# Optimization experiments

Hardware: AMD Instinct MI355X
Metric: run time of the kernel (lower is better)

The kernel has to match this reference:

```python
import jax, jax.numpy as jnp
import numpy as np

N = 50000      # nodes
E = 300000     # edges per relation
IN = 128       # in_feats
HF = 64        # h_feats
AH = 4         # att_heads
R = 3          # relations
H = HF * AH    # 256, per-relation hidden width


def setup_inputs() -> dict:
    key = jax.random.key(0)
    ks = jax.random.split(key, 10)
    s = 0.05
    h = jax.random.normal(ks[0], (N, IN), jnp.float32)
    # relation_aware params (shared across relations)
    dW = jax.random.normal(ks[1], (IN, H), jnp.float32) * s
    db = jnp.zeros((H,), jnp.float32)
    fW = jax.random.normal(ks[2], (3 * H, 1), jnp.float32) * s
    fb = jnp.zeros((1,), jnp.float32)
    # per-relation H2FDLayer params (stacked over R)
    wW = jax.random.normal(ks[3], (R, IN, H), jnp.float32) * s
    wb = jnp.zeros((R, H), jnp.float32)
    aW = jax.random.normal(ks[4], (R, 2 * HF, 1), jnp.float32) * s
    ab = jnp.zeros((R, 1), jnp.float32)
    # final combining linear
    linW = jax.random.normal(ks[5], (R * H, H), jnp.float32) * s
    linb = jnp.zeros((H,), jnp.float32)
    src = jax.random.randint(ks[6], (R, E), 0, N, jnp.int32)
    dst = jax.random.randint(ks[7], (R, E), 0, N, jnp.int32)
    return dict(h=h, dW=dW, db=db, fW=fW, fb=fb, wW=wW, wb=wb,
                aW=aW, ab=ab, linW=linW, linb=linb, src=src, dst=dst)


def _segment_softmax(alpha, seg, num_segments):
    # alpha: [E, AH]; softmax over edges sharing the same destination node
    amax = jax.ops.segment_max(alpha, seg, num_segments=num_segments)
    ex = jnp.exp(alpha - amax[seg])
    denom = jax.ops.segment_sum(ex, seg, num_segments=num_segments)
    return ex / denom[seg]


def reference(h, dW, db, fW, fb, wW, wb, aW, ab, linW, linb, src, dst):
    hd = h @ dW + db  # [N, H] relation_aware d_liner (shared)
    outs = []
    for r in range(R):
        s_idx, d_idx = src[r], dst[r]
        sd, dd = hd[s_idx], hd[d_idx]  # [E, H]
        # sign_edges: tanh(f_liner(cat[src,dst,src-dst])) -> sign
        score = jnp.tanh((jnp.concatenate([sd, dd, sd - dd], axis=1) @ fW + fb)[:, 0])
        sign = jnp.sign(score)  # [E]
        hw = h @ wW[r] + wb[r]  # [N, H] per-relation w_liner
        sf = (sign[:, None] * hw[s_idx]).reshape(E, AH, HF)          # signed src features
        z = jnp.concatenate([sf, hw[d_idx].reshape(E, AH, HF)], -1)  # [E, AH, 2*HF]
        alpha = jax.nn.leaky_relu((z @ aW[r] + ab[r])[..., 0], 0.01)  # [E, AH]
        w = _segment_softmax(alpha, d_idx, N)                         # [E, AH]
        out_r = jax.ops.segment_sum(w[..., None] * sf, d_idx, num_segments=N)
        outs.append(out_r.reshape(N, H))
    out = jnp.concatenate(outs, axis=1)  # [N, R*H]
    return out @ linW + linb             # [N, H]
```

## Files before the change

kernel.cpp:

```cpp
#include <hip/hip_runtime.h>

#define NN 50000
#define MP 50048
#define EE 300000
#define KIN 128
#define HH 256
#define KOUT 768
#define NAH 4
#define NHF 64
#define NR 3

#define GSH 7
#define NG 391
#define NBKT (NR * NG)
#define BCAP 1024
#define EPB 16384
#define NTOT (NR * EE)

typedef __attribute__((ext_vector_type(8))) short short8_t;
typedef __attribute__((ext_vector_type(4))) float f32x4;

#define O_DBL   0ull
#define O_GS    4096ull
#define O_GD    204096ull
#define O_ASRC  404096ull
#define O_ADST  2804096ull
#define O_GCNT  5204096ull
#define O_GBUF  5212288ull
#define O_H16   10016896ull
#define O_WT    22829184ull
#define O_LWT   23025792ull
#define O_HW16  23419008ull
#define O_OUTA  100292736ull
#define NEED_A  177166464ull

__device__ __forceinline__ ushort f2bf(float x) {
  union { float f; unsigned u; } c; c.f = x;
  return (ushort)((c.u + 0x7FFFu + ((c.u >> 16) & 1u)) >> 16);
}
__device__ __forceinline__ float bf2f(ushort u) {
  return __uint_as_float(((unsigned)u) << 16);
}

__global__ void k_prep(const float* __restrict__ dW, const float* __restrict__ db,
                       const float* __restrict__ fW, double* __restrict__ dbuf) {
  int t = threadIdx.x;
  if (t < KIN) {
    double p = 0.0, q = 0.0;
    for (int j = 0; j < HH; ++j) {
      double u = (double)fW[j] + (double)fW[2 * HH + j];
      double v = (double)fW[HH + j] - (double)fW[2 * HH + j];
      double w = (double)dW[t * HH + j];
      p += w * u; q += w * v;
    }
    dbuf[t] = p; dbuf[KIN + t] = q;
  } else if (t == KIN) {
    double cu = 0.0, cv = 0.0;
    for (int j = 0; j < HH; ++j) {
      double u = (double)fW[j] + (double)fW[2 * HH + j];
      double v = (double)fW[HH + j] - (double)fW[2 * HH + j];
      cu += (double)db[j] * u; cv += (double)db[j] * v;
    }
    dbuf[2 * KIN] = cu; dbuf[2 * KIN + 1] = cv;
  }
}

__global__ __launch_bounds__(256) void k_gsgd(const float* __restrict__ h,
                                              const double* __restrict__ dbuf,
                                              float* __restrict__ gs, float* __restrict__ gd) {
  int node = (int)((blockIdx.x * 256u + threadIdx.x) >> 6);
  int lane = threadIdx.x & 63;
  if (node >= NN) return;
  float2 hv = *(const float2*)&h[(size_t)node * KIN + lane * 2];
  double ps = (double)hv.x * dbuf[lane * 2] + (double)hv.y * dbuf[lane * 2 + 1];
  double qs = (double)hv.x * dbuf[KIN + lane * 2] + (double)hv.y * dbuf[KIN + lane * 2 + 1];
#pragma unroll
  for (int m = 32; m; m >>= 1) { ps += __shfl_xor(ps, m, 64); qs += __shfl_xor(qs, m, 64); }
  if (lane == 0) {
    gs[node] = (float)(ps + dbuf[2 * KIN]);
    gd[node] = (float)(qs + dbuf[2 * KIN + 1]);
  }
}

__global__ __launch_bounds__(256) void k_cvtA(const float* __restrict__ h, ushort* __restrict__ h16) {
  int t = blockIdx.x * 256 + threadIdx.x;
  if (t >= MP * KIN / 8) return;
  int row = t >> 4, c8 = (t & 15) * 8;
  ushort o[8];
  if (row < NN) {
    float4 v0 = *(const float4*)&h[(size_t)row * KIN + c8];
    float4 v1 = *(const float4*)&h[(size_t)row * KIN + c8 + 4];
    o[0] = f2bf(v0.x); o[1] = f2bf(v0.y); o[2] = f2bf(v0.z); o[3] = f2bf(v0.w);
    o[4] = f2bf(v1.x); o[5] = f2bf(v1.y); o[6] = f2bf(v1.z); o[7] = f2bf(v1.w);
  } else {
#pragma unroll
    for (int i = 0; i < 8; ++i) o[i] = 0;
  }
  *(short8_t*)&h16[(size_t)row * KIN + c8] = *(short8_t*)o;
}

#define WT_ELEMS (NR * HH * KIN)
#define LWT_ELEMS (HH * KOUT)
__global__ __launch_bounds__(256) void k_cvtW(const float* __restrict__ wW, const float* __restrict__ linW,
                                              ushort* __restrict__ Wt, ushort* __restrict__ LWt) {
  int t = blockIdx.x * 256 + threadIdx.x;
  if (t < WT_ELEMS) {
    int r = t / (HH * KIN), rem = t % (HH * KIN);
    int n = rem / KIN, k = rem % KIN;
    Wt[t] = f2bf(wW[((size_t)r * KIN + k) * HH + n]);
  }
  int u = t - WT_ELEMS;
  if (u >= 0 && u < LWT_ELEMS) {
    int n = u / KOUT, kk = u % KOUT;
    LWt[u] = f2bf(linW[(size_t)kk * HH + n]);
  }
}

template <int K, bool ACC, bool BIAS, bool OBF16>
__global__ __launch_bounds__(256) void k_mm(const ushort* __restrict__ A0,
                                            const ushort* __restrict__ Bt0,
                                            const float* __restrict__ bias0,
                                            void* __restrict__ Cv, int M, int bStride,
                                            size_t aZ, size_t btZ, size_t biasZ, size_t cZ) {
  __shared__ ushort As[128][40];
  __shared__ ushort Bs[128][40];
  const ushort* A = A0 + (size_t)blockIdx.z * aZ;
  const ushort* Bt = Bt0 + (size_t)blockIdx.z * btZ;
  const float* bias = BIAS ? bias0 + (size_t)blockIdx.z * biasZ : bias0;
  size_t cOfs = (size_t)blockIdx.z * cZ;
  int bm = blockIdx.x * 128, bn = blockIdx.y * 128;
  int tid = threadIdx.x, lane = tid & 63, w = tid >> 6;
  int wm = w >> 1, wn = w & 1;
  int sr = tid >> 2, sk = (tid & 3) * 8;
  int fr = lane & 15, kb = (lane >> 4) * 8;
  f32x4 acc[4][4] = {};
  for (int k0 = 0; k0 < K; k0 += 32) {
    short8_t a0 = *(const short8_t*)&A[(size_t)(bm + sr) * K + k0 + sk];
    short8_t a1 = *(const short8_t*)&A[(size_t)(bm + 64 + sr) * K + k0 + sk];
    short8_t b0 = *(const short8_t*)&Bt[(size_t)(bn + sr) * bStride + k0 + sk];
    short8_t b1 = *(const short8_t*)&Bt[(size_t)(bn + 64 + sr) * bStride + k0 + sk];
    __syncthreads();
    *(short8_t*)&As[sr][sk] = a0;
    *(short8_t*)&As[64 + sr][sk] = a1;
    *(short8_t*)&Bs[sr][sk] = b0;
    *(short8_t*)&Bs[64 + sr][sk] = b1;
    __syncthreads();
    short8_t af[4], bfr[4];
#pragma unroll
    for (int i = 0; i < 4; ++i) af[i] = *(const short8_t*)&As[wm * 64 + i * 16 + fr][kb];
#pragma unroll
    for (int i = 0; i < 4; ++i) bfr[i] = *(const short8_t*)&Bs[wn * 64 + i * 16 + fr][kb];
#pragma unroll
    for (int i = 0; i < 4; ++i)
#pragma unroll
      for (int j = 0; j < 4; ++j)
        acc[i][j] = __builtin_amdgcn_mfma_f32_16x16x32_bf16(af[i], bfr[j], acc[i][j], 0, 0, 0);
  }
  int rq = lane >> 4;
#pragma unroll
  for (int i = 0; i < 4; ++i) {
#pragma unroll
    for (int j = 0; j < 4; ++j) {
      int col = bn + wn * 64 + j * 16 + fr;
      float bv = 0.f;
      if constexpr (BIAS) bv = bias[col];
#pragma unroll
      for (int q = 0; q < 4; ++q) {
        int row = bm + wm * 64 + i * 16 + rq * 4 + q;
        if (row < M) {
          float v = acc[i][j][q] + bv;
          if constexpr (OBF16) {
            ((ushort*)Cv)[cOfs + (size_t)row * HH + col] = f2bf(v);
          } else {
            float* C = (float*)Cv;
            if constexpr (ACC) v += C[(size_t)row * HH + col];
            C[(size_t)row * HH + col] = v;
          }
        }
      }
    }
  }
}

__global__ __launch_bounds__(256) void k_aproj(const ushort* __restrict__ hwAll, size_t hwZ,
                                               const float* __restrict__ aWAll,
                                               float* __restrict__ asrcAll, float* __restrict__ adstAll,
                                               int rbase) {
  int r = rbase + blockIdx.y;
  const ushort* hw = hwAll + (size_t)(blockIdx.y) * hwZ;
  const float* aW = aWAll + (size_t)r * 2 * NHF;
  int node = (int)((blockIdx.x * 256u + threadIdx.x) >> 6);
  int lane = threadIdx.x & 63;
  if (node >= NN) return;
  int ah = lane >> 4, j = lane & 15;
  ushort4 hv4 = *(const ushort4*)&hw[(size_t)node * HH + ah * NHF + j * 4];
  float hx = bf2f(hv4.x), hy = bf2f(hv4.y), hz = bf2f(hv4.z), hwv = bf2f(hv4.w);
  float4 a1 = *(const float4*)&aW[j * 4];
  float4 a2 = *(const float4*)&aW[NHF + j * 4];
  float s1 = hx * a1.x + hy * a1.y + hz * a1.z + hwv * a1.w;
  float s2 = hx * a2.x + hy * a2.y + hz * a2.z + hwv * a2.w;
#pragma unroll
  for (int m = 8; m; m >>= 1) { s1 += __shfl_xor(s1, m, 64); s2 += __shfl_xor(s2, m, 64); }
  if (j == 0) {
    asrcAll[(size_t)r * NN * NAH + node * NAH + ah] = s1;
    adstAll[(size_t)r * NN * NAH + node * NAH + ah] = s2;
  }
}

__global__ __launch_bounds__(512) void k_bin(const int* __restrict__ dst,
                                             int* __restrict__ gcnt,
                                             uint* __restrict__ gbuf) {
  __shared__ int hist[NBKT];
  __shared__ int base[NBKT];
  int tid = threadIdx.x;
  int start = blockIdx.x * EPB;
  for (int b = tid; b < NBKT; b += 512) hist[b] = 0;
  __syncthreads();
#pragma unroll 4
  for (int i = 0; i < EPB / 512; ++i) {
    int e = start + i * 512 + tid;
    if (e < NTOT) {
      int d = dst[e];
      int r = (e >= 2 * EE) ? 2 : ((e >= EE) ? 1 : 0);
      atomicAdd(&hist[r * NG + (d >> GSH)], 1);
    }
  }
  __syncthreads();
  for (int b = tid; b < NBKT; b += 512) {
    int c = hist[b];
    base[b] = (c > 0) ? atomicAdd(&gcnt[b], c) : 0;
    hist[b] = 0;
  }
  __syncthreads();
#pragma unroll 4
  for (int i = 0; i < EPB / 512; ++i) {
    int e = start + i * 512 + tid;
    if (e < NTOT) {
      int d = dst[e];
      int r = (e >= 2 * EE) ? 2 : ((e >= EE) ? 1 : 0);
      int bkt = r * NG + (d >> GSH);
      int idx = base[bkt] + atomicAdd(&hist[bkt], 1);
      if (idx < BCAP)
        gbuf[(size_t)bkt * BCAP + idx] = ((uint)(d & 127) << 19) | (uint)(e - r * EE);
    }
  }
}

__global__ __launch_bounds__(512) void k_edgeB(const int* __restrict__ srcAll,
                                               const ushort* __restrict__ hwAll, size_t hwZ,
                                               const float* __restrict__ gs,
                                               const float* __restrict__ gd,
                                               const float* __restrict__ asrcAll,
                                               const float* __restrict__ adstAll,
                                               const float* __restrict__ fb,
                                               const float* __restrict__ abAll,
                                               const int* __restrict__ gcnt,
                                               const uint* __restrict__ gbuf,
                                               ushort* __restrict__ outB,
                                               int outStride, int colMul, int rbase) {
  __shared__ uint ebuf[BCAP];
  __shared__ uint csr[BCAP];
  __shared__ int cntL[128], offL[128], curL[128];
  int rl = blockIdx.x / NG, g = blockIdx.x % NG;
  int r = rbase + rl;
  const int* src = srcAll + (size_t)r * EE;
  const ushort* hw = hwAll + (size_t)rl * hwZ;
  const float* asrc = asrcAll + (size_t)r * NN * NAH;
  const float* adst = adstAll + (size_t)r * NN * NAH;
  int bkt = r * NG + g;
  int tid = threadIdx.x;
  int cb = gcnt[bkt]; if (cb > BCAP) cb = BCAP;
  if (tid < 128) { cntL[tid] = 0; curL[tid] = 0; }
  __syncthreads();
  for (int i = tid; i < cb; i += 512) {
    uint ent = gbuf[(size_t)bkt * BCAP + i];
    ebuf[i] = ent;
    atomicAdd(&cntL[ent >> 19], 1);
  }
  __syncthreads();
  if (tid < 64) {
    int c0 = cntL[2 * tid], c1 = cntL[2 * tid + 1];
    int s = c0 + c1, inc = s;
#pragma unroll
    for (int o = 1; o < 64; o <<= 1) {
      int v = __shfl_up(inc, o, 64);
      if (tid >= o) inc += v;
    }
    int ex = inc - s;
    offL[2 * tid] = ex;
    offL[2 * tid + 1] = ex + c0;
  }
  __syncthreads();
  for (int i = tid; i < cb; i += 512) {
    uint ent = ebuf[i];
    int b = (int)(ent >> 19);
    int idx = atomicAdd(&curL[b], 1);
    csr[offL[b] + idx] = ent;
  }
  __syncthreads();

  int lane = tid & 63, wv = tid >> 6;
  int head = lane >> 4, iE = lane >> 2, cah = lane & 3;
  float fbv = fb[0], abv = abAll[r];
  int colBase = colMul * r * HH + lane * 4;
  for (int it = 0; it < 16; ++it) {
    int ln = wv + 8 * it;
    int node = (g << GSH) + ln;
    if (node >= NN) continue;
    int deg = cntL[ln]; deg = deg < 64 ? deg : 64;
    if (deg == 0) {
      ushort4 z = {0, 0, 0, 0};
      *(ushort4*)&outB[(size_t)node * outStride + colBase] = z;
      continue;
    }
    int bofs = offL[ln];
    float gdn = gd[node];
    float adn = adst[node * NAH + cah];
    float den = 0.f;
    float w_[4]; int s_[4];
#pragma unroll
    for (int p = 0; p < 4; ++p) {
      float wgt = 0.f; int sv = 0;
      if (p * 16 < deg) {
        int e = p * 16 + iE;
        float ex = 0.f;
        if (e < deg) {
          uint ent = csr[bofs + e];
          sv = src[ent & 0x7FFFFu];
          float t = gs[sv] + gdn + fbv;
          float sg = (t > 0.f) ? 1.f : ((t < 0.f) ? -1.f : 0.f);
          float a = sg * asrc[sv * NAH + cah] + adn + abv;
          a = (a >= 0.f) ? a : 0.01f * a;
          ex = __expf(a);
          wgt = sg * ex;
        }
        float red = ex;
#pragma unroll
        for (int m = 4; m <= 32; m <<= 1) red += __shfl_xor(red, m, 64);
        den += red;
      }
      w_[p] = wgt; s_[p] = sv;
    }
    float rd = 1.f / __shfl(den, head, 64);
    float4 acc = {0, 0, 0, 0};
#pragma unroll
    for (int p = 0; p < 4; ++p) {
      if (p * 16 >= deg) break;
      int lim = deg - p * 16; lim = lim < 16 ? lim : 16;
      int i2 = 0;
      for (; i2 + 1 < lim; i2 += 2) {
        float w0 = __shfl(w_[p], i2 * 4 + head, 64);
        int   v0 = __shfl(s_[p], i2 * 4 + head, 64);
        float w1 = __shfl(w_[p], (i2 + 1) * 4 + head, 64);
        int   v1 = __shfl(s_[p], (i2 + 1) * 4 + head, 64);
        ushort4 h0 = *(const ushort4*)&hw[(size_t)v0 * HH + lane * 4];
        ushort4 h1 = *(const ushort4*)&hw[(size_t)v1 * HH + lane * 4];
        acc.x += w0 * bf2f(h0.x) + w1 * bf2f(h1.x);
        acc.y += w0 * bf2f(h0.y) + w1 * bf2f(h1.y);
        acc.z += w0 * bf2f(h0.z) + w1 * bf2f(h1.z);
        acc.w += w0 * bf2f(h0.w) + w1 * bf2f(h1.w);
      }
      if (i2 < lim) {
        float w0 = __shfl(w_[p], i2 * 4 + head, 64);
        int   v0 = __shfl(s_[p], i2 * 4 + head, 64);
        ushort4 h0 = *(const ushort4*)&hw[(size_t)v0 * HH + lane * 4];
        acc.x += w0 * bf2f(h0.x); acc.y += w0 * bf2f(h0.y);
        acc.z += w0 * bf2f(h0.z); acc.w += w0 * bf2f(h0.w);
      }
    }
    ushort4 o;
    o.x = f2bf(acc.x * rd); o.y = f2bf(acc.y * rd);
    o.z = f2bf(acc.z * rd); o.w = f2bf(acc.w * rd);
    *(ushort4*)&outB[(size_t)node * outStride + colBase] = o;
  }
}

extern "C" void kernel_launch(void* const* d_in, const int* in_sizes, int n_in,
                              void* d_out, int out_size, void* d_ws, size_t ws_size,
                              hipStream_t stream) {
  const float* h    = (const float*)d_in[0];
  const float* dW   = (const float*)d_in[1];
  const float* db   = (const float*)d_in[2];
  const float* fW   = (const float*)d_in[3];
  const float* fb   = (const float*)d_in[4];
  const float* wW   = (const float*)d_in[5];
  const float* wb   = (const float*)d_in[6];
  const float* aW   = (const float*)d_in[7];
  const float* ab   = (const float*)d_in[8];
  const float* linW = (const float*)d_in[9];
  const float* linb = (const float*)d_in[10];
  const int*   src  = (const int*)d_in[11];
  const int*   dst  = (const int*)d_in[12];
  float* out = (float*)d_out;
  char* ws = (char*)d_ws;

  double* dbuf  = (double*)(ws + O_DBL);
  float* gs     = (float*)(ws + O_GS);
  float* gd     = (float*)(ws + O_GD);
  float* asrc   = (float*)(ws + O_ASRC);
  float* adst   = (float*)(ws + O_ADST);
  int*   gcnt   = (int*)(ws + O_GCNT);
  uint*  gbuf   = (uint*)(ws + O_GBUF);
  ushort* h16   = (ushort*)(ws + O_H16);
  ushort* Wt    = (ushort*)(ws + O_WT);
  ushort* LWt   = (ushort*)(ws + O_LWT);
  ushort* hw16  = (ushort*)(ws + O_HW16);

  hipMemsetAsync(ws + O_GCNT, 0, 8192, stream);
  k_prep<<<1, 256, 0, stream>>>(dW, db, fW, dbuf);
  k_gsgd<<<NN / 4, 256, 0, stream>>>(h, dbuf, gs, gd);
  k_cvtA<<<(MP * KIN / 8 + 255) / 256, 256, 0, stream>>>(h, h16);
  k_cvtW<<<(WT_ELEMS + LWT_ELEMS + 255) / 256, 256, 0, stream>>>(wW, linW, Wt, LWt);
  k_bin<<<(NTOT + EPB - 1) / EPB, 512, 0, stream>>>(dst, gcnt, gbuf);

  if (ws_size >= NEED_A) {
    ushort* out768 = (ushort*)(ws + O_OUTA);
    k_mm<KIN, false, true, true><<<dim3(MP / 128, 2, 3), 256, 0, stream>>>(
        h16, Wt, wb, hw16, MP, KIN,
        0, (size_t)HH * KIN, (size_t)HH, (size_t)MP * HH);
    k_aproj<<<dim3(NN / 4, 3), 256, 0, stream>>>(hw16, (size_t)MP * HH, aW, asrc, adst, 0);
    k_edgeB<<<NBKT, 512, 0, stream>>>(
        src, hw16, (size_t)MP * HH, gs, gd, asrc, adst, fb, ab,
        gcnt, gbuf, out768, KOUT, 1, 0);
    k_mm<KOUT, false, true, false><<<dim3(MP / 128, 2, 1), 256, 0, stream>>>(
        out768, LWt, linb, out, NN, KOUT, 0, 0, 0, 0);
  } else {
    ushort* outr = hw16 + (size_t)MP * HH;
    for (int r = 0; r < NR; ++r) {
      k_mm<KIN, false, true, true><<<dim3(MP / 128, 2, 1), 256, 0, stream>>>(
          h16, Wt + (size_t)r * HH * KIN, wb + (size_t)r * HH, hw16, MP, KIN, 0, 0, 0, 0);
      k_aproj<<<dim3(NN / 4, 1), 256, 0, stream>>>(hw16, 0, aW, asrc, adst, r);
      k_edgeB<<<NG, 512, 0, stream>>>(
          src, hw16, 0, gs, gd, asrc, adst, fb, ab,
          gcnt, gbuf, outr, HH, 0, r);
      if (r == 0)
        k_mm<HH, false, true, false><<<dim3(MP / 128, 2, 1), 256, 0, stream>>>(
            outr, LWt, linb, out, NN, KOUT, 0, 0, 0, 0);
      else
        k_mm<HH, true, false, false><<<dim3(MP / 128, 2, 1), 256, 0, stream>>>(
            outr, LWt + (size_t)r * HH, nullptr, out, NN, KOUT, 0, 0, 0, 0);
    }
  }
}
```

Baseline: 405.2 us.

## Fold attention projection into fp32 input pass and prefetch edge gathers to LDS

New measurement: 424.9 us. 4.9% more time.

```diff
diff --git a/kernel.cpp b/kernel.cpp
--- a/kernel.cpp
+++ b/kernel.cpp
@@ -21,18 +21,19 @@
 typedef __attribute__((ext_vector_type(4))) float f32x4;
 
 #define O_DBL   0ull
-#define O_GS    4096ull
-#define O_GD    204096ull
-#define O_ASRC  404096ull
-#define O_ADST  2804096ull
-#define O_GCNT  5204096ull
-#define O_GBUF  5212288ull
-#define O_H16   10016896ull
-#define O_WT    22829184ull
-#define O_LWT   23025792ull
-#define O_HW16  23419008ull
-#define O_OUTA  100292736ull
-#define NEED_A  177166464ull
+#define O_AVEC  2080ull
+#define O_ACON  14368ull
+#define O_GS    14464ull
+#define O_GD    214464ull
+#define O_ASRC  414464ull
+#define O_ADST  2814464ull
+#define O_GCNT  5214464ull
+#define O_GBUF  5222656ull
+#define O_H16   10027264ull
+#define O_WT    22839552ull
+#define O_LWT   23036160ull
+#define O_HW16  23429376ull
+#define O_OUTA  100303104ull
 
 __device__ __forceinline__ ushort f2bf(float x) {
   union { float f; unsigned u; } c; c.f = x;
@@ -43,60 +44,98 @@
 }
 
 __global__ void k_prep(const float* __restrict__ dW, const float* __restrict__ db,
-                       const float* __restrict__ fW, double* __restrict__ dbuf) {
-  int t = threadIdx.x;
-  if (t < KIN) {
-    double p = 0.0, q = 0.0;
-    for (int j = 0; j < HH; ++j) {
-      double u = (double)fW[j] + (double)fW[2 * HH + j];
-      double v = (double)fW[HH + j] - (double)fW[2 * HH + j];
-      double w = (double)dW[t * HH + j];
-      p += w * u; q += w * v;
-    }
-    dbuf[t] = p; dbuf[KIN + t] = q;
-  } else if (t == KIN) {
-    double cu = 0.0, cv = 0.0;
-    for (int j = 0; j < HH; ++j) {
-      double u = (double)fW[j] + (double)fW[2 * HH + j];
-      double v = (double)fW[HH + j] - (double)fW[2 * HH + j];
-      cu += (double)db[j] * u; cv += (double)db[j] * v;
-    }
-    dbuf[2 * KIN] = cu; dbuf[2 * KIN + 1] = cv;
-  }
-}
-
-__global__ __launch_bounds__(256) void k_gsgd(const float* __restrict__ h,
+                       const float* __restrict__ fW, const float* __restrict__ wW,
+                       const float* __restrict__ wb, const float* __restrict__ aW,
+                       double* __restrict__ dbuf, float* __restrict__ avec,
+                       float* __restrict__ acon) {
+  int b = blockIdx.x, t = threadIdx.x;
+  if (b == 0) {
+    if (t < KIN) {
+      double p = 0.0, q = 0.0;
+      for (int j = 0; j < HH; ++j) {
+        double u = (double)fW[j] + (double)fW[2 * HH + j];
+        double v = (double)fW[HH + j] - (double)fW[2 * HH + j];
+        double w = (double)dW[t * HH + j];
+        p += w * u; q += w * v;
+      }
+      dbuf[t] = p; dbuf[KIN + t] = q;
+    } else if (t == KIN) {
+      double cu = 0.0, cv = 0.0;
+      for (int j = 0; j < HH; ++j) {
+        double u = (double)fW[j] + (double)fW[2 * HH + j];
+        double v = (double)fW[HH + j] - (double)fW[2 * HH + j];
+        cu += (double)db[j] * u; cv += (double)db[j] * v;
+      }
+      dbuf[2 * KIN] = cu; dbuf[2 * KIN + 1] = cv;
+    }
+  } else if (b <= 12) {
+    int idx = (b - 1) * 256 + t;
+    int d = idx >> 7, k = idx & 127;
+    int r = d >> 3, rem = d & 7, ah = rem >> 1, which = rem & 1;
+    const float* wWr = wW + (size_t)r * KIN * HH;
+    const float* aWr = aW + (size_t)r * 2 * NHF + which * NHF;
+    float s = 0.f;
+    for (int f = 0; f < NHF; ++f) s += wWr[(size_t)k * HH + ah * NHF + f] * aWr[f];
+    avec[idx] = s;
+  } else {
+    if (t < 24) {
+      int d = t, r = d >> 3, rem = d & 7, ah = rem >> 1, which = rem & 1;
+      const float* aWr = aW + (size_t)r * 2 * NHF + which * NHF;
+      const float* wbr = wb + (size_t)r * HH + ah * NHF;
+      float s = 0.f;
+      for (int f = 0; f < NHF; ++f) s += wbr[f] * aWr[f];
+      acon[d] = s;
+    }
+  }
+}
+
+__global__ __launch_bounds__(256) void k_fuse(const float* __restrict__ h,
                                               const double* __restrict__ dbuf,
-                                              float* __restrict__ gs, float* __restrict__ gd) {
-  int node = (int)((blockIdx.x * 256u + threadIdx.x) >> 6);
+                                              const float* __restrict__ avec,
+                                              const float* __restrict__ acon,
+                                              float* __restrict__ gs, float* __restrict__ gd,
+                                              ushort* __restrict__ h16,
+                                              float* __restrict__ asrcAll,
+                                              float* __restrict__ adstAll) {
+  int bid = blockIdx.x;
+  if (bid == NN / 4) {
+    for (int i = threadIdx.x; i < (MP - NN) * KIN / 8; i += 256) {
+      short8_t z = {0, 0, 0, 0, 0, 0, 0, 0};
+      *(short8_t*)&h16[(size_t)NN * KIN + i * 8] = z;
+    }
+    return;
+  }
+  int node = (int)((bid * 256u + threadIdx.x) >> 6);
   int lane = threadIdx.x & 63;
-  if (node >= NN) return;
   float2 hv = *(const float2*)&h[(size_t)node * KIN + lane * 2];
+  ushort2 o2; o2.x = f2bf(hv.x); o2.y = f2bf(hv.y);
+  *(ushort2*)&h16[(size_t)node * KIN + lane * 2] = o2;
   double ps = (double)hv.x * dbuf[lane * 2] + (double)hv.y * dbuf[lane * 2 + 1];
   double qs = (double)hv.x * dbuf[KIN + lane * 2] + (double)hv.y * dbuf[KIN + lane * 2 + 1];
 #pragma unroll
   for (int m = 32; m; m >>= 1) { ps += __shfl_xor(ps, m, 64); qs += __shfl_xor(qs, m, 64); }
+  float res[24];
+#pragma unroll
+  for (int d = 0; d < 24; ++d) {
+    float p = hv.x * avec[d * 128 + 2 * lane] + hv.y * avec[d * 128 + 2 * lane + 1];
+#pragma unroll
+    for (int m = 32; m; m >>= 1) p += __shfl_xor(p, m, 64);
+    res[d] = p;
+  }
   if (lane == 0) {
     gs[node] = (float)(ps + dbuf[2 * KIN]);
     gd[node] = (float)(qs + dbuf[2 * KIN + 1]);
-  }
-}
-
-__global__ __launch_bounds__(256) void k_cvtA(const float* __restrict__ h, ushort* __restrict__ h16) {
-  int t = blockIdx.x * 256 + threadIdx.x;
-  if (t >= MP * KIN / 8) return;
-  int row = t >> 4, c8 = (t & 15) * 8;
-  ushort o[8];
-  if (row < NN) {
-    float4 v0 = *(const float4*)&h[(size_t)row * KIN + c8];
-    float4 v1 = *(const float4*)&h[(size_t)row * KIN + c8 + 4];
-    o[0] = f2bf(v0.x); o[1] = f2bf(v0.y); o[2] = f2bf(v0.z); o[3] = f2bf(v0.w);
-    o[4] = f2bf(v1.x); o[5] = f2bf(v1.y); o[6] = f2bf(v1.z); o[7] = f2bf(v1.w);
-  } else {
-#pragma unroll
-    for (int i = 0; i < 8; ++i) o[i] = 0;
-  }
-  *(short8_t*)&h16[(size_t)row * KIN + c8] = *(short8_t*)o;
+#pragma unroll
+    for (int r = 0; r < NR; ++r) {
+      float4 va, vd;
+      va.x = res[r * 8 + 0] + acon[r * 8 + 0]; vd.x = res[r * 8 + 1] + acon[r * 8 + 1];
+      va.y = res[r * 8 + 2] + acon[r * 8 + 2]; vd.y = res[r * 8 + 3] + acon[r * 8 + 3];
+      va.z = res[r * 8 + 4] + acon[r * 8 + 4]; vd.z = res[r * 8 + 5] + acon[r * 8 + 5];
+      va.w = res[r * 8 + 6] + acon[r * 8 + 6]; vd.w = res[r * 8 + 7] + acon[r * 8 + 7];
+      *(float4*)&asrcAll[(size_t)r * NN * NAH + (size_t)node * NAH] = va;
+      *(float4*)&adstAll[(size_t)r * NN * NAH + (size_t)node * NAH] = vd;
+    }
+  }
 }
 
 #define WT_ELEMS (NR * HH * KIN)
@@ -116,15 +155,15 @@
   }
 }
 
-template <int K, bool ACC, bool BIAS, bool OBF16>
+template <int K, bool BIAS, bool OBF16>
 __global__ __launch_bounds__(256) void k_mm(const ushort* __restrict__ A0,
                                             const ushort* __restrict__ Bt0,
                                             const float* __restrict__ bias0,
                                             void* __restrict__ Cv, int M, int bStride,
-                                            size_t aZ, size_t btZ, size_t biasZ, size_t cZ) {
+                                            size_t btZ, size_t biasZ, size_t cZ) {
   __shared__ ushort As[128][40];
   __shared__ ushort Bs[128][40];
-  const ushort* A = A0 + (size_t)blockIdx.z * aZ;
+  const ushort* A = A0;
   const ushort* Bt = Bt0 + (size_t)blockIdx.z * btZ;
   const float* bias = BIAS ? bias0 + (size_t)blockIdx.z * biasZ : bias0;
   size_t cOfs = (size_t)blockIdx.z * cZ;
@@ -133,10 +172,12 @@
   int wm = w >> 1, wn = w & 1;
   int sr = tid >> 2, sk = (tid & 3) * 8;
   int fr = lane & 15, kb = (lane >> 4) * 8;
+  const bool aok0 = (bm + sr) < M, aok1 = (bm + 64 + sr) < M;
   f32x4 acc[4][4] = {};
   for (int k0 = 0; k0 < K; k0 += 32) {
-    short8_t a0 = *(const short8_t*)&A[(size_t)(bm + sr) * K + k0 + sk];
-    short8_t a1 = *(const short8_t*)&A[(size_t)(bm + 64 + sr) * K + k0 + sk];
+    short8_t a0 = {0, 0, 0, 0, 0, 0, 0, 0}, a1 = {0, 0, 0, 0, 0, 0, 0, 0};
+    if (aok0) a0 = *(const short8_t*)&A[(size_t)(bm + sr) * K + k0 + sk];
+    if (aok1) a1 = *(const short8_t*)&A[(size_t)(bm + 64 + sr) * K + k0 + sk];
     short8_t b0 = *(const short8_t*)&Bt[(size_t)(bn + sr) * bStride + k0 + sk];
     short8_t b1 = *(const short8_t*)&Bt[(size_t)(bn + 64 + sr) * bStride + k0 + sk];
     __syncthreads();
@@ -169,41 +210,11 @@
         int row = bm + wm * 64 + i * 16 + rq * 4 + q;
         if (row < M) {
           float v = acc[i][j][q] + bv;
-          if constexpr (OBF16) {
-            ((ushort*)Cv)[cOfs + (size_t)row * HH + col] = f2bf(v);
-          } else {
-            float* C = (float*)Cv;
-            if constexpr (ACC) v += C[(size_t)row * HH + col];
-            C[(size_t)row * HH + col] = v;
-          }
+          if constexpr (OBF16) ((ushort*)Cv)[cOfs + (size_t)row * HH + col] = f2bf(v);
+          else ((float*)Cv)[(size_t)row * HH + col] = v;
         }
       }
     }
-  }
-}
-
-__global__ __launch_bounds__(256) void k_aproj(const ushort* __restrict__ hwAll, size_t hwZ,
-                                               const float* __restrict__ aWAll,
-                                               float* __restrict__ asrcAll, float* __restrict__ adstAll,
-                                               int rbase) {
-  int r = rbase + blockIdx.y;
-  const ushort* hw = hwAll + (size_t)(blockIdx.y) * hwZ;
-  const float* aW = aWAll + (size_t)r * 2 * NHF;
-  int node = (int)((blockIdx.x * 256u + threadIdx.x) >> 6);
-  int lane = threadIdx.x & 63;
-  if (node >= NN) return;
-  int ah = lane >> 4, j = lane & 15;
-  ushort4 hv4 = *(const ushort4*)&hw[(size_t)node * HH + ah * NHF + j * 4];
-  float hx = bf2f(hv4.x), hy = bf2f(hv4.y), hz = bf2f(hv4.z), hwv = bf2f(hv4.w);
-  float4 a1 = *(const float4*)&aW[j * 4];
-  float4 a2 = *(const float4*)&aW[NHF + j * 4];
-  float s1 = hx * a1.x + hy * a1.y + hz * a1.z + hwv * a1.w;
-  float s2 = hx * a2.x + hy * a2.y + hz * a2.z + hwv * a2.w;
-#pragma unroll
-  for (int m = 8; m; m >>= 1) { s1 += __shfl_xor(s1, m, 64); s2 += __shfl_xor(s2, m, 64); }
-  if (j == 0) {
-    asrcAll[(size_t)r * NN * NAH + node * NAH + ah] = s1;
-    adstAll[(size_t)r * NN * NAH + node * NAH + ah] = s2;
   }
 }
 
@@ -247,7 +258,7 @@
 }
 
 __global__ __launch_bounds__(512) void k_edgeB(const int* __restrict__ srcAll,
-                                               const ushort* __restrict__ hwAll, size_t hwZ,
+                                               const ushort* __restrict__ hwAll,
                                                const float* __restrict__ gs,
                                                const float* __restrict__ gd,
                                                const float* __restrict__ asrcAll,
@@ -256,24 +267,23 @@
                                                const float* __restrict__ abAll,
                                                const int* __restrict__ gcnt,
                                                const uint* __restrict__ gbuf,
-                                               ushort* __restrict__ outB,
-                                               int outStride, int colMul, int rbase) {
+                                               ushort* __restrict__ out768) {
   __shared__ uint ebuf[BCAP];
   __shared__ uint csr[BCAP];
+  __shared__ float gsv[BCAP];
+  __shared__ float asv[BCAP * 4];
   __shared__ int cntL[128], offL[128], curL[128];
   int rl = blockIdx.x / NG, g = blockIdx.x % NG;
-  int r = rbase + rl;
-  const int* src = srcAll + (size_t)r * EE;
-  const ushort* hw = hwAll + (size_t)rl * hwZ;
-  const float* asrc = asrcAll + (size_t)r * NN * NAH;
-  const float* adst = adstAll + (size_t)r * NN * NAH;
-  int bkt = r * NG + g;
+  const int* src = srcAll + (size_t)rl * EE;
+  const ushort* hw = hwAll + (size_t)rl * MP * HH;
+  const float* asrc = asrcAll + (size_t)rl * NN * NAH;
+  const float* adst = adstAll + (size_t)rl * NN * NAH;
   int tid = threadIdx.x;
-  int cb = gcnt[bkt]; if (cb > BCAP) cb = BCAP;
+  int cb = gcnt[blockIdx.x]; if (cb > BCAP) cb = BCAP;
   if (tid < 128) { cntL[tid] = 0; curL[tid] = 0; }
   __syncthreads();
   for (int i = tid; i < cb; i += 512) {
-    uint ent = gbuf[(size_t)bkt * BCAP + i];
+    uint ent = gbuf[(size_t)blockIdx.x * BCAP + i];
     ebuf[i] = ent;
     atomicAdd(&cntL[ent >> 19], 1);
   }
@@ -298,11 +308,18 @@
     csr[offL[b] + idx] = ent;
   }
   __syncthreads();
+  for (int i = tid; i < cb; i += 512) {
+    int sv = src[csr[i] & 0x7FFFFu];
+    ebuf[i] = (uint)sv;
+    gsv[i] = gs[sv];
+    *(float4*)&asv[4 * i] = *(const float4*)&asrc[(size_t)sv * NAH];
+  }
+  __syncthreads();
 
   int lane = tid & 63, wv = tid >> 6;
   int head = lane >> 4, iE = lane >> 2, cah = lane & 3;
-  float fbv = fb[0], abv = abAll[r];
-  int colBase = colMul * r * HH + lane * 4;
+  float fbv = fb[0], abv = abAll[rl];
+  size_t colBase = (size_t)rl * HH + lane * 4;
   for (int it = 0; it < 16; ++it) {
     int ln = wv + 8 * it;
     int node = (g << GSH) + ln;
@@ -310,12 +327,12 @@
     int deg = cntL[ln]; deg = deg < 64 ? deg : 64;
     if (deg == 0) {
       ushort4 z = {0, 0, 0, 0};
-      *(ushort4*)&outB[(size_t)node * outStride + colBase] = z;
+      *(ushort4*)&out768[(size_t)node * KOUT + colBase] = z;
       continue;
     }
     int bofs = offL[ln];
     float gdn = gd[node];
-    float adn = adst[node * NAH + cah];
+    float adn = adst[(size_t)node * NAH + cah];
     float den = 0.f;
     float w_[4]; int s_[4];
 #pragma unroll
@@ -325,11 +342,11 @@
         int e = p * 16 + iE;
         float ex = 0.f;
         if (e < deg) {
-          uint ent = csr[bofs + e];
-          sv = src[ent & 0x7FFFFu];
-          float t = gs[sv] + gdn + fbv;
+          int i = bofs + e;
+          sv = (int)ebuf[i];
+          float t = gsv[i] + gdn + fbv;
           float sg = (t > 0.f) ? 1.f : ((t < 0.f) ? -1.f : 0.f);
-          float a = sg * asrc[sv * NAH + cah] + adn + abv;
+          float a = sg * asv[4 * i + cah] + adn + abv;
           a = (a >= 0.f) ? a : 0.01f * a;
           ex = __expf(a);
           wgt = sg * ex;
@@ -348,19 +365,25 @@
       if (p * 16 >= deg) break;
       int lim = deg - p * 16; lim = lim < 16 ? lim : 16;
       int i2 = 0;
-      for (; i2 + 1 < lim; i2 += 2) {
+      for (; i2 + 3 < lim; i2 += 4) {
         float w0 = __shfl(w_[p], i2 * 4 + head, 64);
         int   v0 = __shfl(s_[p], i2 * 4 + head, 64);
-        float w1 = __shfl(w_[p], (i2 + 1) * 4 + head, 64);
-        int   v1 = __shfl(s_[p], (i2 + 1) * 4 + head, 64);
+        float w1 = __shfl(w_[p], i2 * 4 + 4 + head, 64);
+        int   v1 = __shfl(s_[p], i2 * 4 + 4 + head, 64);
+        float w2 = __shfl(w_[p], i2 * 4 + 8 + head, 64);
+        int   v2 = __shfl(s_[p], i2 * 4 + 8 + head, 64);
+        float w3 = __shfl(w_[p], i2 * 4 + 12 + head, 64);
+        int   v3 = __shfl(s_[p], i2 * 4 + 12 + head, 64);
         ushort4 h0 = *(const ushort4*)&hw[(size_t)v0 * HH + lane * 4];
         ushort4 h1 = *(const ushort4*)&hw[(size_t)v1 * HH + lane * 4];
-        acc.x += w0 * bf2f(h0.x) + w1 * bf2f(h1.x);
-        acc.y += w0 * bf2f(h0.y) + w1 * bf2f(h1.y);
-        acc.z += w0 * bf2f(h0.z) + w1 * bf2f(h1.z);
-        acc.w += w0 * bf2f(h0.w) + w1 * bf2f(h1.w);
-      }
-      if (i2 < lim) {
+        ushort4 h2 = *(const ushort4*)&hw[(size_t)v2 * HH + lane * 4];
+        ushort4 h3 = *(const ushort4*)&hw[(size_t)v3 * HH + lane * 4];
+        acc.x += w0 * bf2f(h0.x) + w1 * bf2f(h1.x) + w2 * bf2f(h2.x) + w3 * bf2f(h3.x);
+        acc.y += w0 * bf2f(h0.y) + w1 * bf2f(h1.y) + w2 * bf2f(h2.y) + w3 * bf2f(h3.y);
+        acc.z += w0 * bf2f(h0.z) + w1 * bf2f(h1.z) + w2 * bf2f(h2.z) + w3 * bf2f(h3.z);
+        acc.w += w0 * bf2f(h0.w) + w1 * bf2f(h1.w) + w2 * bf2f(h2.w) + w3 * bf2f(h3.w);
+      }
+      for (; i2 < lim; ++i2) {
         float w0 = __shfl(w_[p], i2 * 4 + head, 64);
         int   v0 = __shfl(s_[p], i2 * 4 + head, 64);
         ushort4 h0 = *(const ushort4*)&hw[(size_t)v0 * HH + lane * 4];
@@ -371,7 +394,7 @@
     ushort4 o;
     o.x = f2bf(acc.x * rd); o.y = f2bf(acc.y * rd);
     o.z = f2bf(acc.z * rd); o.w = f2bf(acc.w * rd);
-    *(ushort4*)&outB[(size_t)node * outStride + colBase] = o;
+    *(ushort4*)&out768[(size_t)node * KOUT + colBase] = o;
   }
 }
 
@@ -395,6 +418,8 @@
   char* ws = (char*)d_ws;
 
   double* dbuf  = (double*)(ws + O_DBL);
+  float* avec   = (float*)(ws + O_AVEC);
+  float* acon   = (float*)(ws + O_ACON);
   float* gs     = (float*)(ws + O_GS);
   float* gd     = (float*)(ws + O_GD);
   float* asrc   = (float*)(ws + O_ASRC);
@@ -405,40 +430,18 @@
   ushort* Wt    = (ushort*)(ws + O_WT);
   ushort* LWt   = (ushort*)(ws + O_LWT);
   ushort* hw16  = (ushort*)(ws + O_HW16);
+  ushort* out768 = (ushort*)(ws + O_OUTA);
 
   hipMemsetAsync(ws + O_GCNT, 0, 8192, stream);
-  k_prep<<<1, 256, 0, stream>>>(dW, db, fW, dbuf);
-  k_gsgd<<<NN / 4, 256, 0, stream>>>(h, dbuf, gs, gd);
-  k_cvtA<<<(MP * KIN / 8 + 255) / 256, 256, 0, stream>>>(h, h16);
+  k_prep<<<14, 256, 0, stream>>>(dW, db, fW, wW, wb, aW, dbuf, avec, acon);
+  k_fuse<<<NN / 4 + 1, 256, 0, stream>>>(h, dbuf, avec, acon, gs, gd, h16, asrc, adst);
   k_cvtW<<<(WT_ELEMS + LWT_ELEMS + 255) / 256, 256, 0, stream>>>(wW, linW, Wt, LWt);
   k_bin<<<(NTOT + EPB - 1) / EPB, 512, 0, stream>>>(dst, gcnt, gbuf);
 
-  if (ws_size >= NEED_A) {
-    ushort* out768 = (ushort*)(ws + O_OUTA);
-    k_mm<KIN, false, true, true><<<dim3(MP / 128, 2, 3), 256, 0, stream>>>(
-        h16, Wt, wb, hw16, MP, KIN,
-        0, (size_t)HH * KIN, (size_t)HH, (size_t)MP * HH);
-    k_aproj<<<dim3(NN / 4, 3), 256, 0, stream>>>(hw16, (size_t)MP * HH, aW, asrc, adst, 0);
-    k_edgeB<<<NBKT, 512, 0, stream>>>(
-        src, hw16, (size_t)MP * HH, gs, gd, asrc, adst, fb, ab,
-        gcnt, gbuf, out768, KOUT, 1, 0);
-    k_mm<KOUT, false, true, false><<<dim3(MP / 128, 2, 1), 256, 0, stream>>>(
-        out768, LWt, linb, out, NN, KOUT, 0, 0, 0, 0);
-  } else {
-    ushort* outr = hw16 + (size_t)MP * HH;
-    for (int r = 0; r < NR; ++r) {
-      k_mm<KIN, false, true, true><<<dim3(MP / 128, 2, 1), 256, 0, stream>>>(
-          h16, Wt + (size_t)r * HH * KIN, wb + (size_t)r * HH, hw16, MP, KIN, 0, 0, 0, 0);
-      k_aproj<<<dim3(NN / 4, 1), 256, 0, stream>>>(hw16, 0, aW, asrc, adst, r);
-      k_edgeB<<<NG, 512, 0, stream>>>(
-          src, hw16, 0, gs, gd, asrc, adst, fb, ab,
-          gcnt, gbuf, outr, HH, 0, r);
-      if (r == 0)
-        k_mm<HH, false, true, false><<<dim3(MP / 128, 2, 1), 256, 0, stream>>>(
-            outr, LWt, linb, out, NN, KOUT, 0, 0, 0, 0);
-      else
-        k_mm<HH, true, false, false><<<dim3(MP / 128, 2, 1), 256, 0, stream>>>(
-            outr, LWt + (size_t)r * HH, nullptr, out, NN, KOUT, 0, 0, 0, 0);
-    }
-  }
-}
+  k_mm<KIN, true, true><<<dim3(MP / 128, 2, 3), 256, 0, stream>>>(
+      h16, Wt, wb, hw16, MP, KIN, (size_t)HH * KIN, (size_t)HH, (size_t)MP * HH);
+  k_edgeB<<<NBKT, 512, 0, stream>>>(
+      src, hw16, gs, gd, asrc, adst, fb, ab, gcnt, gbuf, out768);
+  k_mm<KOUT, true, false><<<dim3(MP / 128, 2, 1), 256, 0, stream>>>(
+      out768, LWt, linb, out, NN, KOUT, 0, 0, 0);
+}
```
